# Performance work log

Measured on AMD Instinct MI355X. Metric: run time of the kernel, lower is better.

The kernel has to match this reference:

```python
import jax, jax.numpy as jnp
import numpy as np

M, K, D = 8, 512, 64


def setup_inputs() -> dict:
    key = jax.random.key(0)
    k1, k2 = jax.random.split(key)
    logits = jax.random.normal(k1, (8, 2048, M * K), dtype=jnp.float32)
    embeddings = jax.random.normal(k2, (M, K, D), dtype=jnp.float32)
    return {"logits": logits, "embeddings": embeddings}


def reference(logits, embeddings):
    # Training path, relax=False: softmax over codes, hard one-hot argmax,
    # straight-through estimator, then per-split codebook contraction.
    B, T = logits.shape[0], logits.shape[1]
    x = logits.reshape(B * T, M, K)          # (N, M, K)
    p = jax.nn.softmax(x, axis=-1)           # softmax over K codes per split
    idx = jnp.argmax(p, axis=-1)             # (N, M) int
    z_hard = jax.nn.one_hot(idx, K, dtype=p.dtype)
    # straight-through: forward = z_hard, backward flows through p
    z = jax.lax.stop_gradient(z_hard - p) + p
    # per-split codebook lookup expressed as the original bmm:
    # z.transpose(0,1).bmm(embeddings).transpose(0,1) == einsum nmk,mkd->nmd
    qs = jnp.einsum("nmk,mkd->nmd", z, embeddings)  # (N, M, D)
    quantized_stack = qs.reshape(B, T, M, D)
    quantized = quantized_stack.reshape(B, T, M * D)
    encoding_indices = idx.reshape(B, T, M)
    return quantized, quantized_stack, encoding_indices
```

## Files before the change

### kernel.cpp

```cpp
#include <hip/hip_runtime.h>


#define MM 8
#define KK 512
#define DD 64

typedef float f32x4 __attribute__((ext_vector_type(4)));

__device__ inline void task_argmax(f32x4 a, f32x4 b, int lane, float& best, int& bidx) {
    int k0 = lane * 4;
    best = a.x; bidx = k0;
    if (a.y > best) { best = a.y; bidx = k0 + 1; }
    if (a.z > best) { best = a.z; bidx = k0 + 2; }
    if (a.w > best) { best = a.w; bidx = k0 + 3; }
    int k1 = 256 + lane * 4;
    if (b.x > best) { best = b.x; bidx = k1;     }
    if (b.y > best) { best = b.y; bidx = k1 + 1; }
    if (b.z > best) { best = b.z; bidx = k1 + 2; }
    if (b.w > best) { best = b.w; bidx = k1 + 3; }
}

__global__ __launch_bounds__(256) void hardem_fwd(
    const float* __restrict__ logits,
    const float* __restrict__ emb,
    float* __restrict__ out)
{
    const int wave = threadIdx.x >> 6;
    const int lane = threadIdx.x & 63;
    const int wid  = blockIdx.x * 4 + wave;
    const int t0   = wid * 2;
    const int t1   = t0 + 1;

    const f32x4* s0 = (const f32x4*)(logits + (size_t)t0 * KK);
    const f32x4* s1 = (const f32x4*)(logits + (size_t)t1 * KK);
    f32x4 a0 = __builtin_nontemporal_load(&s0[lane]);
    f32x4 b0 = __builtin_nontemporal_load(&s0[64 + lane]);
    f32x4 a1 = __builtin_nontemporal_load(&s1[lane]);
    f32x4 b1 = __builtin_nontemporal_load(&s1[64 + lane]);

    float v0, v1; int i0, i1;
    task_argmax(a0, b0, lane, v0, i0);
    task_argmax(a1, b1, lane, v1, i1);

    #pragma unroll
    for (int mask = 1; mask < 64; mask <<= 1) {
        float o0 = __shfl_xor(v0, mask, 64);
        int   j0 = __shfl_xor(i0, mask, 64);
        float o1 = __shfl_xor(v1, mask, 64);
        int   j1 = __shfl_xor(i1, mask, 64);
        if (o0 > v0 || (o0 == v0 && j0 < i0)) { v0 = o0; i0 = j0; }
        if (o1 > v1 || (o1 == v1 && j1 < i1)) { v1 = o1; i1 = j1; }
    }

    const int m0 = t0 & (MM - 1);
    const int m1 = t1 & (MM - 1);

    float e0 = emb[((size_t)m0 * KK + (size_t)i0) * DD + lane];
    float e1 = emb[((size_t)m1 * KK + (size_t)i1) * DD + lane];

    const size_t q0 = (size_t)t0 * DD + lane;
    const size_t q1 = (size_t)t1 * DD + lane;
    __builtin_nontemporal_store(e0, &out[q0]);
    __builtin_nontemporal_store(e1, &out[q1]);
    __builtin_nontemporal_store(e0, &out[8388608 + q0]);
    __builtin_nontemporal_store(e1, &out[8388608 + q1]);

    if (lane < 2)
        out[16777216 + (size_t)t0 + lane] = (float)(lane ? i1 : i0);
}

extern "C" void kernel_launch(void* const* d_in, const int* in_sizes, int n_in,
                              void* d_out, int out_size, void* d_ws, size_t ws_size,
                              hipStream_t stream) {
    const float* logits = (const float*)d_in[0];
    const float* emb    = (const float*)d_in[1];
    float* out          = (float*)d_out;

    hardem_fwd<<<16384, 256, 0, stream>>>(logits, emb, out);
}
```

Before: 58.55 us.

## Process 16 rows per wave with software-pipelined prefetch of logits

Each wave now loops over 8 iterations of two rows, prefetching the next pair of logit rows while reducing the current pair. The grid shrinks from 16384 to 2048 blocks to match. The aim is to hide global load latency and cut launch and scheduling overhead, in exchange for fewer resident waves to cover memory latency and higher register use.

```diff
diff --git a/kernel.cpp b/kernel.cpp
--- a/kernel.cpp
+++ b/kernel.cpp
@@ -4,6 +4,7 @@
 #define MM 8
 #define KK 512
 #define DD 64
+#define ITERS 8
 
 typedef float f32x4 __attribute__((ext_vector_type(4)));
 
@@ -28,45 +29,57 @@
     const int wave = threadIdx.x >> 6;
     const int lane = threadIdx.x & 63;
     const int wid  = blockIdx.x * 4 + wave;
-    const int t0   = wid * 2;
-    const int t1   = t0 + 1;
+    const int base = wid * (2 * ITERS);
 
-    const f32x4* s0 = (const f32x4*)(logits + (size_t)t0 * KK);
-    const f32x4* s1 = (const f32x4*)(logits + (size_t)t1 * KK);
-    f32x4 a0 = __builtin_nontemporal_load(&s0[lane]);
-    f32x4 b0 = __builtin_nontemporal_load(&s0[64 + lane]);
-    f32x4 a1 = __builtin_nontemporal_load(&s1[lane]);
-    f32x4 b1 = __builtin_nontemporal_load(&s1[64 + lane]);
-
-    float v0, v1; int i0, i1;
-    task_argmax(a0, b0, lane, v0, i0);
-    task_argmax(a1, b1, lane, v1, i1);
+    const f32x4* p0 = (const f32x4*)(logits + (size_t)(base + 0) * KK);
+    const f32x4* p1 = (const f32x4*)(logits + (size_t)(base + 1) * KK);
+    f32x4 A0 = __builtin_nontemporal_load(&p0[lane]);
+    f32x4 B0 = __builtin_nontemporal_load(&p0[64 + lane]);
+    f32x4 A1 = __builtin_nontemporal_load(&p1[lane]);
+    f32x4 B1 = __builtin_nontemporal_load(&p1[64 + lane]);
 
     #pragma unroll
-    for (int mask = 1; mask < 64; mask <<= 1) {
-        float o0 = __shfl_xor(v0, mask, 64);
-        int   j0 = __shfl_xor(i0, mask, 64);
-        float o1 = __shfl_xor(v1, mask, 64);
-        int   j1 = __shfl_xor(i1, mask, 64);
-        if (o0 > v0 || (o0 == v0 && j0 < i0)) { v0 = o0; i0 = j0; }
-        if (o1 > v1 || (o1 == v1 && j1 < i1)) { v1 = o1; i1 = j1; }
+    for (int it = 0; it < ITERS; ++it) {
+        const int t0 = base + it * 2;
+
+        f32x4 nA0, nB0, nA1, nB1;
+        if (it + 1 < ITERS) {
+            const f32x4* q0 = (const f32x4*)(logits + (size_t)(t0 + 2) * KK);
+            const f32x4* q1 = (const f32x4*)(logits + (size_t)(t0 + 3) * KK);
+            nA0 = __builtin_nontemporal_load(&q0[lane]);
+            nB0 = __builtin_nontemporal_load(&q0[64 + lane]);
+            nA1 = __builtin_nontemporal_load(&q1[lane]);
+            nB1 = __builtin_nontemporal_load(&q1[64 + lane]);
+        }
+
+        float v0, v1; int i0, i1;
+        task_argmax(A0, B0, lane, v0, i0);
+        task_argmax(A1, B1, lane, v1, i1);
+
+        #pragma unroll
+        for (int mask = 1; mask < 64; mask <<= 1) {
+            float o0 = __shfl_xor(v0, mask, 64);  int j0 = __shfl_xor(i0, mask, 64);
+            float o1 = __shfl_xor(v1, mask, 64);  int j1 = __shfl_xor(i1, mask, 64);
+            if (o0 > v0 || (o0 == v0 && j0 < i0)) { v0 = o0; i0 = j0; }
+            if (o1 > v1 || (o1 == v1 && j1 < i1)) { v1 = o1; i1 = j1; }
+        }
+
+        const int m0 = (t0 + 0) & (MM - 1);
+        const int m1 = (t0 + 1) & (MM - 1);
+        float e0 = emb[((size_t)m0 * KK + (size_t)i0) * DD + lane];
+        float e1 = emb[((size_t)m1 * KK + (size_t)i1) * DD + lane];
+
+        const size_t q0 = (size_t)t0 * DD + lane;
+        __builtin_nontemporal_store(e0, &out[q0]);
+        __builtin_nontemporal_store(e1, &out[q0 + DD]);
+        __builtin_nontemporal_store(e0, &out[8388608 + q0]);
+        __builtin_nontemporal_store(e1, &out[8388608 + q0 + DD]);
+
+        if (lane < 2)
+            out[16777216 + (size_t)t0 + lane] = (float)(lane ? i1 : i0);
+
+        A0 = nA0; B0 = nB0; A1 = nA1; B1 = nB1;
     }
-
-    const int m0 = t0 & (MM - 1);
-    const int m1 = t1 & (MM - 1);
-
-    float e0 = emb[((size_t)m0 * KK + (size_t)i0) * DD + lane];
-    float e1 = emb[((size_t)m1 * KK + (size_t)i1) * DD + lane];
-
-    const size_t q0 = (size_t)t0 * DD + lane;
-    const size_t q1 = (size_t)t1 * DD + lane;
-    __builtin_nontemporal_store(e0, &out[q0]);
-    __builtin_nontemporal_store(e1, &out[q1]);
-    __builtin_nontemporal_store(e0, &out[8388608 + q0]);
-    __builtin_nontemporal_store(e1, &out[8388608 + q1]);
-
-    if (lane < 2)
-        out[16777216 + (size_t)t0 + lane] = (float)(lane ? i1 : i0);
 }
 
 extern "C" void kernel_launch(void* const* d_in, const int* in_sizes, int n_in,
@@ -76,5 +89,5 @@
     const float* emb    = (const float*)d_in[1];
     float* out          = (float*)d_out;
 
-    hardem_fwd<<<16384, 256, 0, stream>>>(logits, emb, out);
+    hardem_fwd<<<2048, 256, 0, stream>>>(logits, emb, out);
 }
```

After: 64.97 us. 11.0% more time.

## Split argmax and embedding scatter into two kernels with vectorized stores

Applied to the files above, without the earlier changes.

Splits the fused kernel in two. The first kernel computes per-row argmax and writes only the indices. The second reads those indices back and copies embedding rows into both outputs with 128-bit vector stores. The aim is to keep the bandwidth-heavy logits pass free of dependent gather latency and to widen the output stores. The cost is a second launch, a round-trip of the indices through memory, and a serial dependency between the two passes.

```diff
diff --git a/kernel.cpp b/kernel.cpp
--- a/kernel.cpp
+++ b/kernel.cpp
@@ -20,19 +20,17 @@
     if (b.w > best) { best = b.w; bidx = k1 + 3; }
 }
 
-__global__ __launch_bounds__(256) void hardem_fwd(
+__global__ __launch_bounds__(256) void hardem_argmax(
     const float* __restrict__ logits,
-    const float* __restrict__ emb,
     float* __restrict__ out)
 {
     const int wave = threadIdx.x >> 6;
     const int lane = threadIdx.x & 63;
     const int wid  = blockIdx.x * 4 + wave;
     const int t0   = wid * 2;
-    const int t1   = t0 + 1;
 
     const f32x4* s0 = (const f32x4*)(logits + (size_t)t0 * KK);
-    const f32x4* s1 = (const f32x4*)(logits + (size_t)t1 * KK);
+    const f32x4* s1 = (const f32x4*)(logits + (size_t)(t0 + 1) * KK);
     f32x4 a0 = __builtin_nontemporal_load(&s0[lane]);
     f32x4 b0 = __builtin_nontemporal_load(&s0[64 + lane]);
     f32x4 a1 = __builtin_nontemporal_load(&s1[lane]);
@@ -44,29 +42,41 @@
 
     #pragma unroll
     for (int mask = 1; mask < 64; mask <<= 1) {
-        float o0 = __shfl_xor(v0, mask, 64);
-        int   j0 = __shfl_xor(i0, mask, 64);
-        float o1 = __shfl_xor(v1, mask, 64);
-        int   j1 = __shfl_xor(i1, mask, 64);
+        float o0 = __shfl_xor(v0, mask, 64);  int j0 = __shfl_xor(i0, mask, 64);
+        float o1 = __shfl_xor(v1, mask, 64);  int j1 = __shfl_xor(i1, mask, 64);
         if (o0 > v0 || (o0 == v0 && j0 < i0)) { v0 = o0; i0 = j0; }
         if (o1 > v1 || (o1 == v1 && j1 < i1)) { v1 = o1; i1 = j1; }
     }
 
-    const int m0 = t0 & (MM - 1);
-    const int m1 = t1 & (MM - 1);
-
-    float e0 = emb[((size_t)m0 * KK + (size_t)i0) * DD + lane];
-    float e1 = emb[((size_t)m1 * KK + (size_t)i1) * DD + lane];
-
-    const size_t q0 = (size_t)t0 * DD + lane;
-    const size_t q1 = (size_t)t1 * DD + lane;
-    __builtin_nontemporal_store(e0, &out[q0]);
-    __builtin_nontemporal_store(e1, &out[q1]);
-    __builtin_nontemporal_store(e0, &out[8388608 + q0]);
-    __builtin_nontemporal_store(e1, &out[8388608 + q1]);
-
     if (lane < 2)
         out[16777216 + (size_t)t0 + lane] = (float)(lane ? i1 : i0);
+}
+
+__global__ __launch_bounds__(256) void hardem_scatter(
+    const float* __restrict__ emb,
+    float* __restrict__ out)
+{
+    const int wave = threadIdx.x >> 6;
+    const int lane = threadIdx.x & 63;
+    const int wid  = blockIdx.x * 4 + wave;
+    const int base = wid * 4;
+
+    float idxf = 0.0f;
+    if (lane < 4) idxf = out[16777216 + (size_t)base + lane];
+
+    const int g = lane >> 4;
+    const int o = lane & 15;
+    const int idx = (int)__shfl(idxf, g, 64);
+    const int t = base + g;
+    const int m = t & (MM - 1);
+
+    const f32x4* erow = (const f32x4*)(emb + ((size_t)m * KK + (size_t)idx) * DD);
+    f32x4 e = erow[o];
+
+    f32x4* q  = (f32x4*)(out + (size_t)t * DD);
+    f32x4* qs = (f32x4*)(out + 8388608 + (size_t)t * DD);
+    __builtin_nontemporal_store(e, &q[o]);
+    __builtin_nontemporal_store(e, &qs[o]);
 }
 
 extern "C" void kernel_launch(void* const* d_in, const int* in_sizes, int n_in,
@@ -76,5 +86,6 @@
     const float* emb    = (const float*)d_in[1];
     float* out          = (float*)d_out;
 
-    hardem_fwd<<<16384, 256, 0, stream>>>(logits, emb, out);
+    hardem_argmax<<<16384, 256, 0, stream>>>(logits, out);
+    hardem_scatter<<<8192, 256, 0, stream>>>(emb, out);
 }
```

Measured after the change: 56.06 us. 1.04x faster.
